# Kernel optimization log

Hardware: AMD Instinct MI355X
Metric: run time of the kernel (lower is better)

The kernel has to match this reference:

```python
import jax, jax.numpy as jnp
import numpy as np

N_WIRES = 4
N_LAYERS = 2
B = 16384
EPS = 1e-5


def apply_ry(state, wire, theta):
    # state: (B,2,2,2,2) complex64; theta: scalar or (B,)
    st = jnp.moveaxis(state, wire + 1, 1)
    half = jnp.asarray(theta) * 0.5
    c = jnp.cos(half).reshape(-1, 1, 1, 1).astype(state.dtype)
    s = jnp.sin(half).reshape(-1, 1, 1, 1).astype(state.dtype)
    n0 = c * st[:, 0] - s * st[:, 1]
    n1 = s * st[:, 0] + c * st[:, 1]
    return jnp.moveaxis(jnp.stack([n0, n1], axis=1), 1, wire + 1)


def apply_rz(state, wire, theta):
    st = jnp.moveaxis(state, wire + 1, 1)
    half = jnp.asarray(theta) * 0.5
    c = jnp.cos(half)
    s = jnp.sin(half)
    p0 = (c - 1j * s).reshape(-1, 1, 1, 1).astype(state.dtype)
    p1 = (c + 1j * s).reshape(-1, 1, 1, 1).astype(state.dtype)
    return jnp.moveaxis(jnp.stack([p0 * st[:, 0], p1 * st[:, 1]], axis=1), 1, wire + 1)


def apply_cnot(state, ctrl, tgt):
    st = jnp.moveaxis(state, (ctrl + 1, tgt + 1), (1, 2))
    # flip target where control == 1
    st = jnp.concatenate([st[:, :1], st[:, 1:, ::-1]], axis=1)
    return jnp.moveaxis(st, (1, 2), (ctrl + 1, tgt + 1))


def expect_z(state):
    probs = jnp.real(state * jnp.conj(state))  # (B,2,2,2,2)
    exps = []
    for w in range(N_WIRES):
        p = jnp.moveaxis(probs, w + 1, 1)
        exps.append((p[:, 0] - p[:, 1]).sum(axis=(1, 2, 3)))
    return jnp.stack(exps, axis=-1)  # (B,4)


def quanv(x, qparams):
    bsz = x.shape[0]
    # 2x2 patches in row-major loop order: (B, 196, 4) with [p00,p01,p10,p11]
    patches = x.reshape(bsz, 14, 2, 14, 2).transpose(0, 1, 3, 2, 4).reshape(bsz, 196, 4)
    patches = jnp.transpose(patches, (1, 0, 2))  # (196, B, 4)
    state0 = jnp.zeros((bsz, 2, 2, 2, 2), jnp.complex64).at[:, 0, 0, 0, 0].set(1.0)

    def step(state, vals):
        # NOTE: original code never resets the device between patches -> state carries over
        for i in range(N_WIRES):
            state = apply_ry(state, i, vals[:, i])
        for l in range(N_LAYERS):
            for i in range(N_WIRES):
                state = apply_ry(state, i, qparams[l, i, 0])
                state = apply_rz(state, i, qparams[l, i, 1])
            for i in range(N_WIRES - 1):
                state = apply_cnot(state, i, i + 1)
        return state, expect_z(state)

    _, meas = jax.lax.scan(step, state0, patches)  # (196, B, 4)
    return jnp.transpose(meas, (1, 0, 2)).reshape(bsz, 196 * 4)


def batchnorm(h, g, b):
    # training-mode BatchNorm1d: biased batch statistics
    m = h.mean(axis=0)
    v = h.var(axis=0)
    return g * (h - m) / jnp.sqrt(v + EPS) + b


def setup_inputs() -> dict:
    key = jax.random.key(0)
    ks = jax.random.split(key, 6)
    x = jax.random.uniform(ks[0], (B, 28, 28), dtype=jnp.float32)
    qparams = jax.random.normal(ks[1], (N_LAYERS, N_WIRES, 2), dtype=jnp.float32)
    w1 = jax.random.normal(ks[2], (256, 784), dtype=jnp.float32) * 0.03
    w2 = jax.random.normal(ks[3], (256, 256), dtype=jnp.float32) * 0.05
    w3 = jax.random.normal(ks[4], (10, 256), dtype=jnp.float32) * 0.05
    return {
        "x": x, "qparams": qparams,
        "w1": w1, "b1": jnp.zeros((256,), jnp.float32),
        "g1": jnp.ones((256,), jnp.float32), "be1": jnp.zeros((256,), jnp.float32),
        "w2": w2, "b2": jnp.zeros((256,), jnp.float32),
        "g2": jnp.ones((256,), jnp.float32), "be2": jnp.zeros((256,), jnp.float32),
        "w3": w3, "b3": jnp.zeros((10,), jnp.float32),
    }


def reference(x, qparams, w1, b1, g1, be1, w2, b2, g2, be2, w3, b3):
    feats = quanv(x, qparams)                      # (B, 784)
    h = jax.nn.relu(batchnorm(feats @ w1.T + b1, g1, be1))
    h2 = jax.nn.relu(batchnorm(h @ w2.T + b2, g2, be2)) + h
    return jax.nn.log_softmax(h2 @ w3.T + b3, axis=-1)
```

## Files before the change

kernel.cpp:

```cpp
#include <hip/hip_runtime.h>
#include <math.h>

#define BQ 16384
#define KFP 800
#define NH 256
#define NCLS 10

typedef float f32x4 __attribute__((ext_vector_type(4)));
typedef unsigned int u32x2 __attribute__((ext_vector_type(2)));
typedef unsigned int u32x4 __attribute__((ext_vector_type(4)));
typedef __bf16 bf16x8 __attribute__((ext_vector_type(8)));
typedef __bf16 bf16x4 __attribute__((ext_vector_type(4)));


template<int ST>
__device__ __forceinline__ void u_ry(float* sr, float* si, float c, float s) {
#pragma unroll
  for (int i = 0; i < 16; i++) {
    if (i & ST) continue;
    const int j = i | ST;
    const float a0r = sr[i], a0i = si[i], a1r = sr[j], a1i = si[j];
    sr[i] = c * a0r - s * a1r;  si[i] = c * a0i - s * a1i;
    sr[j] = s * a0r + c * a1r;  si[j] = s * a0i + c * a1i;
  }
}
template<int ST>
__device__ __forceinline__ void u_rz(float* sr, float* si, float c, float s) {
#pragma unroll
  for (int i = 0; i < 16; i++) {
    const float pz = (i & ST) ? s : -s;
    const float ar = sr[i], ai = si[i];
    sr[i] = c * ar - pz * ai;
    si[i] = c * ai + pz * ar;
  }
}
template<int SC, int STG>
__device__ __forceinline__ void u_cnot(float* sr, float* si) {
#pragma unroll
  for (int i = 0; i < 16; i++) {
    if (!(i & SC) || (i & STG)) continue;
    const int j = i | STG;
    float t;
    t = sr[i]; sr[i] = sr[j]; sr[j] = t;
    t = si[i]; si[i] = si[j]; si[j] = t;
  }
}

__global__ __launch_bounds__(256) void prep_kernel(
    const float* __restrict__ qp, const float* __restrict__ w1,
    const float* __restrict__ w2, __bf16* __restrict__ Abuf,
    __bf16* __restrict__ w1b, __bf16* __restrict__ w2b,
    float* __restrict__ gs1, float* __restrict__ gs2) {
  const int bid = blockIdx.x;
  const int tid = threadIdx.x;
  if (bid == 0) {
    gs1[tid] = 0.f; gs1[256 + tid] = 0.f;
    gs2[tid] = 0.f; gs2[256 + tid] = 0.f;
    __shared__ float Ur[16][16], Ui[16][16];
    if (tid < 16) {
      float sr[16], si[16];
#pragma unroll
      for (int i = 0; i < 16; i++) { sr[i] = (i == tid) ? 1.f : 0.f; si[i] = 0.f; }
#pragma unroll
      for (int l = 0; l < 2; l++) {
        { const float t = qp[l*8 + 0] * 0.5f; u_ry<8>(sr, si, cosf(t), sinf(t)); }
        { const float t = qp[l*8 + 1] * 0.5f; u_rz<8>(sr, si, cosf(t), sinf(t)); }
        { const float t = qp[l*8 + 2] * 0.5f; u_ry<4>(sr, si, cosf(t), sinf(t)); }
        { const float t = qp[l*8 + 3] * 0.5f; u_rz<4>(sr, si, cosf(t), sinf(t)); }
        { const float t = qp[l*8 + 4] * 0.5f; u_ry<2>(sr, si, cosf(t), sinf(t)); }
        { const float t = qp[l*8 + 5] * 0.5f; u_rz<2>(sr, si, cosf(t), sinf(t)); }
        { const float t = qp[l*8 + 6] * 0.5f; u_ry<1>(sr, si, cosf(t), sinf(t)); }
        { const float t = qp[l*8 + 7] * 0.5f; u_rz<1>(sr, si, cosf(t), sinf(t)); }
        u_cnot<8, 4>(sr, si);
        u_cnot<4, 2>(sr, si);
        u_cnot<2, 1>(sr, si);
      }
#pragma unroll
      for (int r = 0; r < 16; r++) { Ur[r][tid] = sr[r]; Ui[r][tid] = si[r]; }
    }
    __syncthreads();
    for (int f = tid; f < 2048; f += 256) {
      const int m   = f & 7;
      const int row = (f >> 3) & 15;
      const int kg  = (f >> 7) & 3;
      const int hl  = (f >> 9) & 1;
      const int t   = (f >> 10) & 1;
      const int k   = kg * 8 + m;
      const int ri_o  = (row >> 2) & 1;
      const int amp_o = ((row >> 3) & 1) * 8 + t * 4 + (row & 3);
      const int ri_i  = (k >> 3) & 1;
      const int amp_i = ((k >> 4) & 1) * 8 + (m >> 2) * 4 + (m & 3);
      const float u_r = Ur[amp_o][amp_i], u_i = Ui[amp_o][amp_i];
      float v = (ri_o == 0) ? ((ri_i == 0) ? u_r : -u_i)
                            : ((ri_i == 0) ? u_i : u_r);
      if (hl) {
        const __bf16 hb = (__bf16)v;
        v = v - (float)hb;
      }
      Abuf[f] = (__bf16)v;
    }
  } else if (bid <= 256) {
    const int r = bid - 1;
    for (int c = tid; c < KFP; c += 256)
      w1b[r * KFP + c] = (c < 784) ? (__bf16)w1[r * 784 + c] : (__bf16)0.f;
  } else {
    const int base = (bid - 257) * 2048 + tid * 8;
    const float4 v0 = *(const float4*)(w2 + base);
    const float4 v1 = *(const float4*)(w2 + base + 4);
    bf16x8 o = {(__bf16)v0.x, (__bf16)v0.y, (__bf16)v0.z, (__bf16)v0.w,
                (__bf16)v1.x, (__bf16)v1.y, (__bf16)v1.z, (__bf16)v1.w};
    *(bf16x8*)(w2b + base) = o;
  }
}


__device__ __forceinline__ float swz16(float v) {
  return __int_as_float(__builtin_amdgcn_ds_swizzle(__float_as_int(v), 0x401F));
}
__device__ __forceinline__ float pl32(float v, bool r0sel) {
  const u32x2 r = __builtin_amdgcn_permlane32_swap(
      __float_as_uint(v), __float_as_uint(v), false, false);
  return __uint_as_float(r0sel ? r.x : r.y);
}

__global__ __launch_bounds__(256) void quanv_mfma(
    const float* __restrict__ x, const __bf16* __restrict__ Abuf,
    __bf16* __restrict__ feats) {
  const int tid = threadIdx.x;
  const int l = tid & 63;
  const int wv = tid >> 6;
  const int col = l & 15;
  const int kg = l >> 4;
  const int b = blockIdx.x * 64 + wv * 16 + col;
  const float* xb = x + (size_t)b * 784;
  __bf16* fb = feats + (size_t)b * KFP;
  const float sg0 = (l & 32) ? 1.f : -1.f;

  const u32x2 pt = __builtin_amdgcn_permlane32_swap((unsigned)l, (unsigned)l,
                                                    false, false);
  const bool p32r0 = (pt.x == (unsigned)(l ^ 32));

  const bf16x8* Ab = (const bf16x8*)Abuf;
  const bf16x8 A0h = Ab[(0 * 4 + kg) * 16 + col];
  const bf16x8 A0l = Ab[(1 * 4 + kg) * 16 + col];
  const bf16x8 A1h = Ab[(2 * 4 + kg) * 16 + col];
  const bf16x8 A1l = Ab[(3 * 4 + kg) * 16 + col];

  f32x4 c0 = {(kg == 0) ? 1.f : 0.f, 0.f, 0.f, 0.f};
  f32x4 c1 = {0.f, 0.f, 0.f, 0.f};
  const f32x4 z4 = {0.f, 0.f, 0.f, 0.f};

  float cw[4], sw[4];
  auto trig = [&](float2 a, float2 b2) {
    const float h0 = a.x * 0.5f, h1 = a.y * 0.5f;
    const float h2 = b2.x * 0.5f, h3 = b2.y * 0.5f;
    cw[0] = __cosf(h0); sw[0] = __sinf(h0);
    cw[1] = __cosf(h1); sw[1] = __sinf(h1);
    cw[2] = __cosf(h2); sw[2] = __sinf(h2);
    cw[3] = __cosf(h3); sw[3] = __sinf(h3);
  };

  auto meas = [&](__bf16* dst) {
    const float sq0 = c0.x * c0.x, sq1 = c0.y * c0.y;
    const float sq2 = c0.z * c0.z, sq3 = c0.w * c0.w;
    const float sq4 = c1.x * c1.x, sq5 = c1.y * c1.y;
    const float sq6 = c1.z * c1.z, sq7 = c1.w * c1.w;
    const float s01 = sq0 + sq1, s23 = sq2 + sq3;
    const float s45 = sq4 + sq5, s67 = sq6 + sq7;
    const float d01 = sq0 - sq1, d23 = sq2 - sq3;
    const float d45 = sq4 - sq5, d67 = sq6 - sq7;
    const float z3 = (d01 + d23) + (d45 + d67);
    const float z2 = (s01 - s23) + (s45 - s67);
    const float q03 = s01 + s23, q47 = s45 + s67;
    const float z1 = q03 - q47;
    const float T  = q03 + q47;
    const float z3a = z3 + swz16(z3);
    const float z2a = z2 + swz16(z2);
    const float z1a = z1 + swz16(z1);
    const float Ta  = T + swz16(T);
    const float z3f = z3a + pl32(z3a, p32r0);
    const float z2f = z2a + pl32(z2a, p32r0);
    const float z1f = z1a + pl32(z1a, p32r0);
    const float z0f = sg0 * (pl32(Ta, p32r0) - Ta);
    if (kg == 0) {
      bf16x4 o = {(__bf16)z0f, (__bf16)z1f, (__bf16)z2f, (__bf16)z3f};
      *(bf16x4*)dst = o;
    }
  };

  auto step = [&]() {
    float S[8] = {c0.x, c0.y, c0.z, c0.w, c1.x, c1.y, c1.z, c1.w};
#pragma unroll
    for (int j = 0; j < 4; j++) {
      const float a = S[j];
      S[j]     = fmaf(-sw[1], S[4 + j], cw[1] * S[j]);
      S[4 + j] = fmaf( sw[1], a,        cw[1] * S[4 + j]);
    }
#pragma unroll
    for (int base = 0; base < 8; base += 4)
#pragma unroll
      for (int j = 0; j < 2; j++) {
        const int i0 = base + j, i1 = base + j + 2;
        const float a = S[i0];
        S[i0] = fmaf(-sw[2], S[i1], cw[2] * S[i0]);
        S[i1] = fmaf( sw[2], a,     cw[2] * S[i1]);
      }
#pragma unroll
    for (int i0 = 0; i0 < 8; i0 += 2) {
      const float a = S[i0];
      S[i0]     = fmaf(-sw[3], S[i0 + 1], cw[3] * S[i0]);
      S[i0 + 1] = fmaf( sw[3], a,         cw[3] * S[i0 + 1]);
    }
    float P[8];
#pragma unroll
    for (int i = 0; i < 8; i++) P[i] = pl32(S[i], p32r0);
    const float ss0 = sg0 * sw[0];
#pragma unroll
    for (int i = 0; i < 8; i++) S[i] = fmaf(ss0, P[i], cw[0] * S[i]);

    unsigned sb[8], lb[8];
#pragma unroll
    for (int i = 0; i < 8; i++) {
      sb[i] = __float_as_uint(S[i]);
      lb[i] = __float_as_uint(S[i] - __uint_as_float(sb[i] & 0xFFFF0000u));
    }
    u32x4 bh, bl;
#pragma unroll
    for (int j = 0; j < 4; j++) {
      bh[j] = __builtin_amdgcn_perm(sb[2 * j + 1], sb[2 * j], 0x07060302u);
      bl[j] = __builtin_amdgcn_perm(lb[2 * j + 1], lb[2 * j], 0x07060302u);
    }
    const bf16x8 Bh = __builtin_bit_cast(bf16x8, bh);
    const bf16x8 Bl = __builtin_bit_cast(bf16x8, bl);

    const f32x4 p0 = __builtin_amdgcn_mfma_f32_16x16x32_bf16(A0h, Bh, z4, 0, 0, 0);
    const f32x4 q0 = __builtin_amdgcn_mfma_f32_16x16x32_bf16(A0l, Bh, z4, 0, 0, 0);
    const f32x4 r0 = __builtin_amdgcn_mfma_f32_16x16x32_bf16(A0h, Bl, z4, 0, 0, 0);
    const f32x4 p1 = __builtin_amdgcn_mfma_f32_16x16x32_bf16(A1h, Bh, z4, 0, 0, 0);
    const f32x4 q1 = __builtin_amdgcn_mfma_f32_16x16x32_bf16(A1l, Bh, z4, 0, 0, 0);
    const f32x4 r1 = __builtin_amdgcn_mfma_f32_16x16x32_bf16(A1h, Bl, z4, 0, 0, 0);
    c0 = (p0 + q0) + r0;
    c1 = (p1 + q1) + r1;
  };

  {
    const float2 a0 = *(const float2*)(xb);
    const float2 a1 = *(const float2*)(xb + 28);
    trig(a0, a1);
  }
  float2 t0 = *(const float2*)(xb + 2);
  float2 t1 = *(const float2*)(xb + 30);
  int nrr = 0, ncc = 2;
  __bf16* fp = fb;

  for (int it = 0; it < 196; ++it) {
    const float* np = (it < 194) ? (xb + 56 * nrr + 2 * ncc) : xb;
    const float2 n0 = *(const float2*)np;
    const float2 n1 = *(const float2*)(np + 28);
    ncc++;
    if (ncc == 14) { ncc = 0; nrr++; }

    if (it > 0) { meas(fp); fp += 4; }
    step();
    trig(t0, t1);
    t0 = n0; t1 = n1;
  }
  meas(fp);

  if (kg == 0) {
    *(uint4*)(fb + 784) = (uint4){0, 0, 0, 0};
    *(uint4*)(fb + 792) = (uint4){0, 0, 0, 0};
  }
}

#define GBM 128
#define GBN 64
#define GBK 32

__device__ __forceinline__ void gld16(const void* g, void* l) {
  __builtin_amdgcn_global_load_lds(
      (const __attribute__((address_space(1))) unsigned int*)g,
      (__attribute__((address_space(3))) unsigned int*)l, 16, 0, 0);
}

__global__ __launch_bounds__(256) void gemm_bf16_nt(
    const __bf16* __restrict__ A, const __bf16* __restrict__ B,
    const float* __restrict__ bias, float* __restrict__ C,
    int M, int N, int K, float* __restrict__ gstats) {
  __shared__ char lds[24576];
  const int tid = threadIdx.x;
  const int bm = blockIdx.x * GBM;
  const int bn = blockIdx.y * GBN;
  const int NK = K / GBK;
  const size_t lda = (size_t)K * 2;

  const int srow = tid >> 2;
  const int lc16 = tid & 3;
  const int ag0 = lc16 ^ ((srow >> 1) & 3);
  const int ag1 = lc16 ^ (((srow + 64) >> 1) & 3);
  const char* a0p = (const char*)A + (size_t)(bm + srow) * lda + ag0 * 16;
  const char* a1p = (const char*)A + (size_t)(bm + 64 + srow) * lda + ag1 * 16;
  const char* b0p = (const char*)B + (size_t)(bn + srow) * lda + ag0 * 16;

  const int wid = tid >> 6, lane = tid & 63;
  const int wr = wid >> 1, wc = wid & 1;
  const int ln15 = lane & 15, ln4 = lane >> 4;
  int aoff[4], boff[2];
#pragma unroll
  for (int m = 0; m < 4; m++) {
    const int row = wr * 64 + m * 16 + ln15;
    aoff[m] = row * 64 + ((ln4 ^ ((row >> 1) & 3)) * 16);
  }
#pragma unroll
  for (int n = 0; n < 2; n++) {
    const int row = wc * 32 + n * 16 + ln15;
    boff[n] = 16384 + row * 64 + ((ln4 ^ ((row >> 1) & 3)) * 16);
  }

  f32x4 acc[4][2];
#pragma unroll
  for (int m = 0; m < 4; m++)
#pragma unroll
    for (int n = 0; n < 2; n++) acc[m][n] = (f32x4){0.f, 0.f, 0.f, 0.f};

  auto stage = [&](int buf, int kt) {
    const size_t kb = (size_t)kt * GBK * 2;
    char* as = lds + buf * 8192 + tid * 16;
    char* bs = lds + 16384 + buf * 4096 + tid * 16;
    gld16(a0p + kb, as);
    gld16(a1p + kb, as + 4096);
    gld16(b0p + kb, bs);
  };

  stage(0, 0);
  for (int kt = 0; kt < NK; kt++) {
    __syncthreads();
    if (kt + 1 < NK) stage((kt + 1) & 1, kt + 1);
    const int ab = (kt & 1) * 8192, bb = (kt & 1) * 4096;
    bf16x8 af[4], bfr[2];
#pragma unroll
    for (int m = 0; m < 4; m++) af[m] = *(const bf16x8*)(lds + ab + aoff[m]);
#pragma unroll
    for (int n = 0; n < 2; n++) bfr[n] = *(const bf16x8*)(lds + bb + boff[n]);
#pragma unroll
    for (int m = 0; m < 4; m++)
#pragma unroll
      for (int n = 0; n < 2; n++)
        acc[m][n] = __builtin_amdgcn_mfma_f32_16x16x32_bf16(af[m], bfr[n], acc[m][n], 0, 0, 0);
  }

  float csum[2], csq[2];
#pragma unroll
  for (int n = 0; n < 2; n++) {
    const int ccol = bn + wc * 32 + n * 16 + ln15;
    const float bv = bias[ccol];
    float s = 0.f, ss = 0.f;
#pragma unroll
    for (int m = 0; m < 4; m++) {
      const int crow = bm + wr * 64 + m * 16 + ln4 * 4;
#pragma unroll
      for (int r = 0; r < 4; r++) {
        const float v = acc[m][n][r] + bv;
        C[(size_t)(crow + r) * N + ccol] = v;
        s += v; ss += v * v;
      }
    }
    csum[n] = s; csq[n] = ss;
  }
  __syncthreads();
  float* sred = (float*)lds;
#pragma unroll
  for (int n = 0; n < 2; n++) {
    const int slot = wid * 128 + ln4 * 32 + n * 16 + ln15;
    sred[slot] = csum[n];
    sred[512 + slot] = csq[n];
  }
  __syncthreads();
  if (tid < 128) {
    const int colb = tid & 63, which = tid >> 6;
    const int wcc = colb >> 5, c31 = colb & 31;
    float a = 0.f;
    const int base = which * 512 + c31;
#pragma unroll
    for (int w2_ = 0; w2_ < 2; w2_++)
#pragma unroll
      for (int l4 = 0; l4 < 4; l4++)
        a += sred[base + (w2_ * 2 + wcc) * 128 + l4 * 32];
    atomicAdd(&gstats[(bn + colb) * 2 + which], a);
  }
}

__global__ __launch_bounds__(256) void bn_finalize_g(
    const float* __restrict__ gstats, const float* __restrict__ g,
    const float* __restrict__ be, float* __restrict__ ab, float* __restrict__ cb) {
  const int t = threadIdx.x;
  const float s = gstats[t * 2], ss = gstats[t * 2 + 1];
  const float mean = s * (1.f / 16384.f);
  const float var = ss * (1.f / 16384.f) - mean * mean;
  const float rstd = rsqrtf(var + 1e-5f);
  const float a = g[t] * rstd;
  ab[t] = a;
  cb[t] = be[t] - mean * a;
}

__global__ __launch_bounds__(256) void bn_relu_cvt(
    const float* __restrict__ h, __bf16* __restrict__ hb,
    const float* __restrict__ ab, const float* __restrict__ cb) {
  const size_t i = (size_t)blockIdx.x * 256 + threadIdx.x;
  const float4 v = ((const float4*)h)[i];
  const int col = (int)((i * 4) & (NH - 1));
  const float4 a = *(const float4*)(ab + col);
  const float4 c = *(const float4*)(cb + col);
  bf16x4 o = {(__bf16)fmaxf(fmaf(v.x, a.x, c.x), 0.f),
              (__bf16)fmaxf(fmaf(v.y, a.y, c.y), 0.f),
              (__bf16)fmaxf(fmaf(v.z, a.z, c.z), 0.f),
              (__bf16)fmaxf(fmaf(v.w, a.w, c.w), 0.f)};
  *(bf16x4*)(hb + i * 4) = o;
}

__global__ __launch_bounds__(256) void tail_fused(
    const float* __restrict__ h2p, const __bf16* __restrict__ h1b,
    const float* __restrict__ ab, const float* __restrict__ cb,
    const float* __restrict__ w3, const float* __restrict__ b3,
    float* __restrict__ out) {
  __shared__ float w3s[NCLS * NH];
  __shared__ float as[NH], cs[NH];
  for (int i = threadIdx.x; i < NCLS * NH; i += 256) w3s[i] = w3[i];
  as[threadIdx.x] = ab[threadIdx.x];
  cs[threadIdx.x] = cb[threadIdx.x];
  __syncthreads();

  const int m = blockIdx.x * 256 + threadIdx.x;
  const float* hr = h2p + (size_t)m * NH;
  const __bf16* rr = h1b + (size_t)m * NH;
  float acc[NCLS];
#pragma unroll
  for (int n = 0; n < NCLS; n++) acc[n] = b3[n];

  for (int k = 0; k < NH; k += 8) {
    const float4 hv0 = *(const float4*)(hr + k);
    const float4 hv1 = *(const float4*)(hr + k + 4);
    const bf16x8 rv = *(const bf16x8*)(rr + k);
    float v[8] = {hv0.x, hv0.y, hv0.z, hv0.w, hv1.x, hv1.y, hv1.z, hv1.w};
#pragma unroll
    for (int j = 0; j < 8; j++)
      v[j] = fmaxf(fmaf(v[j], as[k + j], cs[k + j]), 0.f) + (float)rv[j];
#pragma unroll
    for (int n = 0; n < NCLS; n++) {
      float d = 0.f;
#pragma unroll
      for (int j = 0; j < 8; j++) d = fmaf(v[j], w3s[n * NH + k + j], d);
      acc[n] += d;
    }
  }

  float mx = acc[0];
#pragma unroll
  for (int n = 1; n < NCLS; n++) mx = fmaxf(mx, acc[n]);
  float se = 0.f;
#pragma unroll
  for (int n = 0; n < NCLS; n++) se += expf(acc[n] - mx);
  const float lse = logf(se) + mx;
#pragma unroll
  for (int n = 0; n < NCLS; n++) out[(size_t)m * NCLS + n] = acc[n] - lse;
}

extern "C" void kernel_launch(void* const* d_in, const int* in_sizes, int n_in,
                              void* d_out, int out_size, void* d_ws, size_t ws_size,
                              hipStream_t stream) {
  const float* x   = (const float*)d_in[0];
  const float* qp  = (const float*)d_in[1];
  const float* w1  = (const float*)d_in[2];
  const float* b1  = (const float*)d_in[3];
  const float* g1  = (const float*)d_in[4];
  const float* be1 = (const float*)d_in[5];
  const float* w2  = (const float*)d_in[6];
  const float* b2  = (const float*)d_in[7];
  const float* g2  = (const float*)d_in[8];
  const float* be2 = (const float*)d_in[9];
  const float* w3  = (const float*)d_in[10];
  const float* b3  = (const float*)d_in[11];
  float* out = (float*)d_out;

  char* w = (char*)d_ws;
  __bf16* feats = (__bf16*)w;
  float*  h1    = (float*)(w + 26214400);
  float*  h2p   = (float*)(w + 42991616);
  __bf16* h1b   = (__bf16*)(w + 59768832);
  __bf16* w1b   = (__bf16*)(w + 68157440);
  __bf16* w2b   = (__bf16*)(w + 68567040);
  float*  gs1   = (float*)(w + 68698112);
  float*  gs2   = (float*)(w + 68700160);
  float*  ab1   = (float*)(w + 68702208);
  float*  cb1   = (float*)(w + 68703232);
  float*  ab2   = (float*)(w + 68704256);
  float*  cb2   = (float*)(w + 68705280);
  __bf16* Abuf  = (__bf16*)(w + 68706304);

  prep_kernel<<<289, 256, 0, stream>>>(qp, w1, w2, Abuf, w1b, w2b, gs1, gs2);
  quanv_mfma<<<BQ / 64, 256, 0, stream>>>(x, Abuf, feats);

  gemm_bf16_nt<<<dim3(BQ / GBM, NH / GBN), 256, 0, stream>>>(
      feats, w1b, b1, h1, BQ, NH, KFP, gs1);
  bn_finalize_g<<<1, 256, 0, stream>>>(gs1, g1, be1, ab1, cb1);
  bn_relu_cvt<<<(BQ * NH / 4) / 256, 256, 0, stream>>>(h1, h1b, ab1, cb1);

  gemm_bf16_nt<<<dim3(BQ / GBM, NH / GBN), 256, 0, stream>>>(
      h1b, w2b, b2, h2p, BQ, NH, NH, gs2);
  bn_finalize_g<<<1, 256, 0, stream>>>(gs2, g2, be2, ab2, cb2);

  tail_fused<<<BQ / 256, 256, 0, stream>>>(h2p, h1b, ab2, cb2, w3, b3, out);
}
```

Measured before the change: 201.0 us.

## Use tangent-form rotations, fold cosine product, chain MFMAs, remap GEMM tiles

The quanvolution step now writes each RY rotation in tangent form (one FMA per amplitude) and folds the product of the four cosines into a single scale applied before the bf16 hi/lo split. This removes many multiplies but adds four divisions per patch, and accuracy suffers when a cosine is near zero. The measurement reductions use a permlane swap sum. The two correction MFMAs are chained through the accumulator, and the loop is peeled and unrolled by two. Separately, the GEMM uses a 1D grid with a swizzled block-to-tile map across XCDs for better cache locality.

```diff
diff --git a/kernel.cpp b/kernel.cpp
--- a/kernel.cpp
+++ b/kernel.cpp
@@ -8,7 +8,6 @@
 
 typedef float f32x4 __attribute__((ext_vector_type(4)));
 typedef unsigned int u32x2 __attribute__((ext_vector_type(2)));
-typedef unsigned int u32x4 __attribute__((ext_vector_type(4)));
 typedef __bf16 bf16x8 __attribute__((ext_vector_type(8)));
 typedef __bf16 bf16x4 __attribute__((ext_vector_type(4)));
 
@@ -117,7 +116,12 @@
 __device__ __forceinline__ float swz16(float v) {
   return __int_as_float(__builtin_amdgcn_ds_swizzle(__float_as_int(v), 0x401F));
 }
-__device__ __forceinline__ float pl32(float v, bool r0sel) {
+__device__ __forceinline__ float plsum(float v) {
+  const u32x2 r = __builtin_amdgcn_permlane32_swap(
+      __float_as_uint(v), __float_as_uint(v), false, false);
+  return __uint_as_float(r.x) + __uint_as_float(r.y);
+}
+__device__ __forceinline__ float plpick(float v, bool r0sel) {
   const u32x2 r = __builtin_amdgcn_permlane32_swap(
       __float_as_uint(v), __float_as_uint(v), false, false);
   return __uint_as_float(r0sel ? r.x : r.y);
@@ -150,14 +154,19 @@
   f32x4 c1 = {0.f, 0.f, 0.f, 0.f};
   const f32x4 z4 = {0.f, 0.f, 0.f, 0.f};
 
-  float cw[4], sw[4];
+  float ts0, tw1, tw2, tw3, gsc;
   auto trig = [&](float2 a, float2 b2) {
     const float h0 = a.x * 0.5f, h1 = a.y * 0.5f;
     const float h2 = b2.x * 0.5f, h3 = b2.y * 0.5f;
-    cw[0] = __cosf(h0); sw[0] = __sinf(h0);
-    cw[1] = __cosf(h1); sw[1] = __sinf(h1);
-    cw[2] = __cosf(h2); sw[2] = __sinf(h2);
-    cw[3] = __cosf(h3); sw[3] = __sinf(h3);
+    const float c0_ = __cosf(h0), s0_ = __sinf(h0);
+    const float c1_ = __cosf(h1), s1_ = __sinf(h1);
+    const float c2_ = __cosf(h2), s2_ = __sinf(h2);
+    const float c3_ = __cosf(h3), s3_ = __sinf(h3);
+    ts0 = sg0 * __fdividef(s0_, c0_);
+    tw1 = __fdividef(s1_, c1_);
+    tw2 = __fdividef(s2_, c2_);
+    tw3 = __fdividef(s3_, c3_);
+    gsc = (c0_ * c1_) * (c2_ * c3_);
   };
 
   auto meas = [&](__bf16* dst) {
@@ -177,11 +186,11 @@
     const float z3a = z3 + swz16(z3);
     const float z2a = z2 + swz16(z2);
     const float z1a = z1 + swz16(z1);
-    const float Ta  = T + swz16(T);
-    const float z3f = z3a + pl32(z3a, p32r0);
-    const float z2f = z2a + pl32(z2a, p32r0);
-    const float z1f = z1a + pl32(z1a, p32r0);
-    const float z0f = sg0 * (pl32(Ta, p32r0) - Ta);
+    const float Ta  = -sg0 * (T + swz16(T));
+    const float z3f = plsum(z3a);
+    const float z2f = plsum(z2a);
+    const float z1f = plsum(z1a);
+    const float z0f = plsum(Ta);
     if (kg == 0) {
       bf16x4 o = {(__bf16)z0f, (__bf16)z1f, (__bf16)z2f, (__bf16)z3f};
       *(bf16x4*)dst = o;
@@ -193,8 +202,8 @@
 #pragma unroll
     for (int j = 0; j < 4; j++) {
       const float a = S[j];
-      S[j]     = fmaf(-sw[1], S[4 + j], cw[1] * S[j]);
-      S[4 + j] = fmaf( sw[1], a,        cw[1] * S[4 + j]);
+      S[j]     = fmaf(-tw1, S[4 + j], S[j]);
+      S[4 + j] = fmaf( tw1, a,        S[4 + j]);
     }
 #pragma unroll
     for (int base = 0; base < 8; base += 4)
@@ -202,65 +211,59 @@
       for (int j = 0; j < 2; j++) {
         const int i0 = base + j, i1 = base + j + 2;
         const float a = S[i0];
-        S[i0] = fmaf(-sw[2], S[i1], cw[2] * S[i0]);
-        S[i1] = fmaf( sw[2], a,     cw[2] * S[i1]);
+        S[i0] = fmaf(-tw2, S[i1], S[i0]);
+        S[i1] = fmaf( tw2, a,     S[i1]);
       }
 #pragma unroll
     for (int i0 = 0; i0 < 8; i0 += 2) {
       const float a = S[i0];
-      S[i0]     = fmaf(-sw[3], S[i0 + 1], cw[3] * S[i0]);
-      S[i0 + 1] = fmaf( sw[3], a,         cw[3] * S[i0 + 1]);
-    }
-    float P[8];
-#pragma unroll
-    for (int i = 0; i < 8; i++) P[i] = pl32(S[i], p32r0);
-    const float ss0 = sg0 * sw[0];
-#pragma unroll
-    for (int i = 0; i < 8; i++) S[i] = fmaf(ss0, P[i], cw[0] * S[i]);
-
-    unsigned sb[8], lb[8];
+      S[i0]     = fmaf(-tw3, S[i0 + 1], S[i0]);
+      S[i0 + 1] = fmaf( tw3, a,         S[i0 + 1]);
+    }
 #pragma unroll
     for (int i = 0; i < 8; i++) {
-      sb[i] = __float_as_uint(S[i]);
-      lb[i] = __float_as_uint(S[i] - __uint_as_float(sb[i] & 0xFFFF0000u));
-    }
-    u32x4 bh, bl;
-#pragma unroll
-    for (int j = 0; j < 4; j++) {
-      bh[j] = __builtin_amdgcn_perm(sb[2 * j + 1], sb[2 * j], 0x07060302u);
-      bl[j] = __builtin_amdgcn_perm(lb[2 * j + 1], lb[2 * j], 0x07060302u);
-    }
-    const bf16x8 Bh = __builtin_bit_cast(bf16x8, bh);
-    const bf16x8 Bl = __builtin_bit_cast(bf16x8, bl);
-
-    const f32x4 p0 = __builtin_amdgcn_mfma_f32_16x16x32_bf16(A0h, Bh, z4, 0, 0, 0);
-    const f32x4 q0 = __builtin_amdgcn_mfma_f32_16x16x32_bf16(A0l, Bh, z4, 0, 0, 0);
-    const f32x4 r0 = __builtin_amdgcn_mfma_f32_16x16x32_bf16(A0h, Bl, z4, 0, 0, 0);
-    const f32x4 p1 = __builtin_amdgcn_mfma_f32_16x16x32_bf16(A1h, Bh, z4, 0, 0, 0);
-    const f32x4 q1 = __builtin_amdgcn_mfma_f32_16x16x32_bf16(A1l, Bh, z4, 0, 0, 0);
-    const f32x4 r1 = __builtin_amdgcn_mfma_f32_16x16x32_bf16(A1h, Bl, z4, 0, 0, 0);
-    c0 = (p0 + q0) + r0;
-    c1 = (p1 + q1) + r1;
+      const float P = plpick(S[i], p32r0);
+      S[i] = fmaf(ts0, P, S[i]);
+    }
+    bf16x8 Bh, Bl;
+#pragma unroll
+    for (int i = 0; i < 8; i++) {
+      const float GS = gsc * S[i];
+      const __bf16 hb = (__bf16)GS;
+      Bh[i] = hb;
+      Bl[i] = (__bf16)(GS - (float)hb);
+    }
+    f32x4 p0 = __builtin_amdgcn_mfma_f32_16x16x32_bf16(A0h, Bh, z4, 0, 0, 0);
+    f32x4 q0 = __builtin_amdgcn_mfma_f32_16x16x32_bf16(A0l, Bh, z4, 0, 0, 0);
+    q0 = __builtin_amdgcn_mfma_f32_16x16x32_bf16(A0h, Bl, q0, 0, 0, 0);
+    f32x4 p1 = __builtin_amdgcn_mfma_f32_16x16x32_bf16(A1h, Bh, z4, 0, 0, 0);
+    f32x4 q1 = __builtin_amdgcn_mfma_f32_16x16x32_bf16(A1l, Bh, z4, 0, 0, 0);
+    q1 = __builtin_amdgcn_mfma_f32_16x16x32_bf16(A1h, Bl, q1, 0, 0, 0);
+    c0 = p0 + q0;
+    c1 = p1 + q1;
   };
 
-  {
-    const float2 a0 = *(const float2*)(xb);
-    const float2 a1 = *(const float2*)(xb + 28);
-    trig(a0, a1);
-  }
-  float2 t0 = *(const float2*)(xb + 2);
-  float2 t1 = *(const float2*)(xb + 30);
-  int nrr = 0, ncc = 2;
+  float2 t0 = *(const float2*)(xb);
+  float2 t1 = *(const float2*)(xb + 28);
+  trig(t0, t1);
+  t0 = *(const float2*)(xb + 2);
+  t1 = *(const float2*)(xb + 30);
+  step();
+  trig(t0, t1);
+  t0 = *(const float2*)(xb + 4);
+  t1 = *(const float2*)(xb + 32);
+  int nrr = 0, ncc = 3;
   __bf16* fp = fb;
 
-  for (int it = 0; it < 196; ++it) {
+#pragma unroll 2
+  for (int it = 1; it < 196; ++it) {
     const float* np = (it < 194) ? (xb + 56 * nrr + 2 * ncc) : xb;
     const float2 n0 = *(const float2*)np;
     const float2 n1 = *(const float2*)(np + 28);
     ncc++;
     if (ncc == 14) { ncc = 0; nrr++; }
 
-    if (it > 0) { meas(fp); fp += 4; }
+    meas(fp); fp += 4;
     step();
     trig(t0, t1);
     t0 = n0; t1 = n1;
@@ -289,8 +292,10 @@
     int M, int N, int K, float* __restrict__ gstats) {
   __shared__ char lds[24576];
   const int tid = threadIdx.x;
-  const int bm = blockIdx.x * GBM;
-  const int bn = blockIdx.y * GBN;
+  const int nwg = gridDim.x;
+  const int sid = (blockIdx.x & 7) * (nwg >> 3) + (blockIdx.x >> 3);
+  const int bm = (sid >> 2) * GBM;
+  const int bn = (sid & 3) * GBN;
   const int NK = K / GBK;
   const size_t lda = (size_t)K * 2;
 
@@ -500,12 +505,12 @@
   prep_kernel<<<289, 256, 0, stream>>>(qp, w1, w2, Abuf, w1b, w2b, gs1, gs2);
   quanv_mfma<<<BQ / 64, 256, 0, stream>>>(x, Abuf, feats);
 
-  gemm_bf16_nt<<<dim3(BQ / GBM, NH / GBN), 256, 0, stream>>>(
+  gemm_bf16_nt<<<(BQ / GBM) * (NH / GBN), 256, 0, stream>>>(
       feats, w1b, b1, h1, BQ, NH, KFP, gs1);
   bn_finalize_g<<<1, 256, 0, stream>>>(gs1, g1, be1, ab1, cb1);
   bn_relu_cvt<<<(BQ * NH / 4) / 256, 256, 0, stream>>>(h1, h1b, ab1, cb1);
 
-  gemm_bf16_nt<<<dim3(BQ / GBM, NH / GBN), 256, 0, stream>>>(
+  gemm_bf16_nt<<<(BQ / GBM) * (NH / GBN), 256, 0, stream>>>(
       h1b, w2b, b2, h2p, BQ, NH, NH, gs2);
   bn_finalize_g<<<1, 256, 0, stream>>>(gs2, g2, be2, ab2, cb2);
 
```

New measurement: 202.4 us. Within noise of the previous version (+0.7%).
